# Kernel tuning notes

Hardware: AMD Instinct MI355X
Metric: run time of the kernel (lower is better)

The kernel has to match this reference:

```python
import jax, jax.numpy as jnp
import numpy as np


def setup_inputs() -> dict:
    key = jax.random.key(0)
    n_class, n_support, n_query, feature_dim = 32, 16, 16, 1024
    n_rows = n_class * n_support + n_query * n_class  # 1024
    data = jax.random.normal(key, (n_rows, feature_dim), dtype=jnp.float32)
    return {"data": data, "n_class": n_class, "n_support": n_support, "n_query": n_query}


def reference(data, n_class, n_support, n_query):
    D = data.shape[-1]
    # support: [n_class, n_support, D]; query: [n_query*n_class, D]
    support = data[: n_class * n_support].reshape(n_class, n_support, D)
    query = data[n_class * n_support :]
    # attention score: tanh(elementwise product) summed over feature dim
    # scores: [Q, n_class, n_support]  (Q = n_query*n_class)
    scores = jnp.tanh(support[None, :, :, :] * query[:, None, None, :]).sum(-1)
    att = jax.nn.softmax(scores, axis=-1)  # softmax over n_support
    # weighted instance pooling -> prototypes per (query, class): [Q, n_class, D]
    proto = jnp.einsum("qcs,csd->qcd", att, support)
    return proto
```

## Files before the change

### kernel.cpp

```cpp
#include <hip/hip_runtime.h>

constexpr int NC = 32, NS = 16, NQ = 512, D = 1024;
constexpr int QPB = 8;

__global__ __launch_bounds__(256, 2)
void proto_attn_kernel(const float* __restrict__ data, float* __restrict__ out) {
    const int c    = blockIdx.x;
    const int qt   = blockIdx.y;
    const int tid  = threadIdx.x;
    const int wave = tid >> 6;
    const int lane = tid & 63;

    __shared__ float4 sup4[NS * (D / 4)];

    const float4* sg = reinterpret_cast<const float4*>(data + (size_t)c * NS * D);
    #pragma unroll
    for (int i = 0; i < 16; ++i)
        sup4[tid + 256 * i] = sg[tid + 256 * i];
    __syncthreads();

    const float K = 2.88539008177792681472f;
    const int q0 = qt * QPB + wave * 2;
    float4 qa[4], qb[4];
    const float4* qg0 = reinterpret_cast<const float4*>(data + (size_t)(NC * NS + q0) * D);
    const float4* qg1 = reinterpret_cast<const float4*>(data + (size_t)(NC * NS + q0 + 1) * D);
    #pragma unroll
    for (int j = 0; j < 4; ++j) {
        float4 t0 = qg0[lane + 64 * j];
        float4 t1 = qg1[lane + 64 * j];
        qa[j] = make_float4(t0.x * K, t0.y * K, t0.z * K, t0.w * K);
        qb[j] = make_float4(t1.x * K, t1.y * K, t1.z * K, t1.w * K);
    }

    float sc0[NS], sc1[NS];
    #pragma unroll
    for (int s = 0; s < NS; ++s) {
        float r0 = 0.f, r1 = 0.f;
        #pragma unroll
        for (int j = 0; j < 4; ++j) {
            float4 sv = sup4[s * (D / 4) + lane + 64 * j];
            r0 += __builtin_amdgcn_rcpf(__builtin_amdgcn_exp2f(sv.x * qa[j].x) + 1.f);
            r0 += __builtin_amdgcn_rcpf(__builtin_amdgcn_exp2f(sv.y * qa[j].y) + 1.f);
            r0 += __builtin_amdgcn_rcpf(__builtin_amdgcn_exp2f(sv.z * qa[j].z) + 1.f);
            r0 += __builtin_amdgcn_rcpf(__builtin_amdgcn_exp2f(sv.w * qa[j].w) + 1.f);
            r1 += __builtin_amdgcn_rcpf(__builtin_amdgcn_exp2f(sv.x * qb[j].x) + 1.f);
            r1 += __builtin_amdgcn_rcpf(__builtin_amdgcn_exp2f(sv.y * qb[j].y) + 1.f);
            r1 += __builtin_amdgcn_rcpf(__builtin_amdgcn_exp2f(sv.z * qb[j].z) + 1.f);
            r1 += __builtin_amdgcn_rcpf(__builtin_amdgcn_exp2f(sv.w * qb[j].w) + 1.f);
        }
        #pragma unroll
        for (int m = 32; m >= 1; m >>= 1) {
            r0 += __shfl_xor(r0, m, 64);
            r1 += __shfl_xor(r1, m, 64);
        }
        sc0[s] = (float)D - 2.f * r0;
        sc1[s] = (float)D - 2.f * r1;
    }

    const float L2E = 1.44269504088896340736f;
    float m0 = sc0[0], m1 = sc1[0];
    #pragma unroll
    for (int s = 1; s < NS; ++s) { m0 = fmaxf(m0, sc0[s]); m1 = fmaxf(m1, sc1[s]); }
    float sum0 = 0.f, sum1 = 0.f;
    #pragma unroll
    for (int s = 0; s < NS; ++s) {
        sc0[s] = __builtin_amdgcn_exp2f((sc0[s] - m0) * L2E);
        sc1[s] = __builtin_amdgcn_exp2f((sc1[s] - m1) * L2E);
        sum0 += sc0[s];
        sum1 += sc1[s];
    }
    const float inv0 = __builtin_amdgcn_rcpf(sum0);
    const float inv1 = __builtin_amdgcn_rcpf(sum1);

    float4 o0[4], o1[4];
    #pragma unroll
    for (int j = 0; j < 4; ++j) {
        o0[j] = make_float4(0.f, 0.f, 0.f, 0.f);
        o1[j] = make_float4(0.f, 0.f, 0.f, 0.f);
    }
    #pragma unroll
    for (int s = 0; s < NS; ++s) {
        const float a0 = sc0[s] * inv0;
        const float a1 = sc1[s] * inv1;
        #pragma unroll
        for (int j = 0; j < 4; ++j) {
            float4 sv = sup4[s * (D / 4) + lane + 64 * j];
            o0[j].x += a0 * sv.x; o0[j].y += a0 * sv.y;
            o0[j].z += a0 * sv.z; o0[j].w += a0 * sv.w;
            o1[j].x += a1 * sv.x; o1[j].y += a1 * sv.y;
            o1[j].z += a1 * sv.z; o1[j].w += a1 * sv.w;
        }
    }
    float4* og0 = reinterpret_cast<float4*>(out + ((size_t)q0 * NC + c) * D);
    float4* og1 = reinterpret_cast<float4*>(out + ((size_t)(q0 + 1) * NC + c) * D);
    #pragma unroll
    for (int j = 0; j < 4; ++j) {
        og0[lane + 64 * j] = o0[j];
        og1[lane + 64 * j] = o1[j];
    }
}

extern "C" void kernel_launch(void* const* d_in, const int* in_sizes, int n_in,
                              void* d_out, int out_size, void* d_ws, size_t ws_size,
                              hipStream_t stream) {
    (void)in_sizes; (void)n_in; (void)out_size; (void)d_ws; (void)ws_size;
    const float* data = (const float*)d_in[0];
    float* out = (float*)d_out;
    dim3 grid(NC, NQ / QPB);
    proto_attn_kernel<<<grid, dim3(256), 0, stream>>>(data, out);
}
```

Before: 153.5 us.

## Stage support features in two halves to halve LDS and raise occupancy

Shared memory drops from 64KB to 32KB by loading the support set in two feature halves. The score pass and the pooling pass each walk both halves, so the second half is reused at the end of scoring and the first half is reloaded from global for pooling. Launch bounds rise from 2 to 4 blocks per CU to take advantage of the smaller LDS footprint. The cost is an extra global reload of half the support, plus two more block barriers. Per-lane partial sums now go into float4 accumulators before the cross-lane reduction.

```diff
diff --git a/kernel.cpp b/kernel.cpp
--- a/kernel.cpp
+++ b/kernel.cpp
@@ -2,8 +2,13 @@
 
 constexpr int NC = 32, NS = 16, NQ = 512, D = 1024;
 constexpr int QPB = 8;
+constexpr int F4H = 128;
 
-__global__ __launch_bounds__(256, 2)
+__device__ __forceinline__ float rcp1p(float t) {
+    return __builtin_amdgcn_rcpf(__builtin_amdgcn_exp2f(t) + 1.f);
+}
+
+__global__ __launch_bounds__(256, 4)
 void proto_attn_kernel(const float* __restrict__ data, float* __restrict__ out) {
     const int c    = blockIdx.x;
     const int qt   = blockIdx.y;
@@ -11,19 +16,15 @@
     const int wave = tid >> 6;
     const int lane = tid & 63;
 
-    __shared__ float4 sup4[NS * (D / 4)];
+    __shared__ float4 sup4[NS * F4H];
 
     const float4* sg = reinterpret_cast<const float4*>(data + (size_t)c * NS * D);
-    #pragma unroll
-    for (int i = 0; i < 16; ++i)
-        sup4[tid + 256 * i] = sg[tid + 256 * i];
-    __syncthreads();
 
     const float K = 2.88539008177792681472f;
     const int q0 = qt * QPB + wave * 2;
+    const float4* qg0 = reinterpret_cast<const float4*>(data + (size_t)(NC * NS + q0) * D);
+    const float4* qg1 = qg0 + 256;
     float4 qa[4], qb[4];
-    const float4* qg0 = reinterpret_cast<const float4*>(data + (size_t)(NC * NS + q0) * D);
-    const float4* qg1 = reinterpret_cast<const float4*>(data + (size_t)(NC * NS + q0 + 1) * D);
     #pragma unroll
     for (int j = 0; j < 4; ++j) {
         float4 t0 = qg0[lane + 64 * j];
@@ -32,22 +33,59 @@
         qb[j] = make_float4(t1.x * K, t1.y * K, t1.z * K, t1.w * K);
     }
 
+    #pragma unroll
+    for (int i = 0; i < 8; ++i) {
+        int idx = tid + 256 * i;
+        sup4[idx] = sg[((idx >> 7) << 8) + (idx & 127)];
+    }
+    __syncthreads();
+
     float sc0[NS], sc1[NS];
     #pragma unroll
     for (int s = 0; s < NS; ++s) {
-        float r0 = 0.f, r1 = 0.f;
+        float4 t0 = make_float4(0.f, 0.f, 0.f, 0.f);
+        float4 t1 = make_float4(0.f, 0.f, 0.f, 0.f);
         #pragma unroll
-        for (int j = 0; j < 4; ++j) {
-            float4 sv = sup4[s * (D / 4) + lane + 64 * j];
-            r0 += __builtin_amdgcn_rcpf(__builtin_amdgcn_exp2f(sv.x * qa[j].x) + 1.f);
-            r0 += __builtin_amdgcn_rcpf(__builtin_amdgcn_exp2f(sv.y * qa[j].y) + 1.f);
-            r0 += __builtin_amdgcn_rcpf(__builtin_amdgcn_exp2f(sv.z * qa[j].z) + 1.f);
-            r0 += __builtin_amdgcn_rcpf(__builtin_amdgcn_exp2f(sv.w * qa[j].w) + 1.f);
-            r1 += __builtin_amdgcn_rcpf(__builtin_amdgcn_exp2f(sv.x * qb[j].x) + 1.f);
-            r1 += __builtin_amdgcn_rcpf(__builtin_amdgcn_exp2f(sv.y * qb[j].y) + 1.f);
-            r1 += __builtin_amdgcn_rcpf(__builtin_amdgcn_exp2f(sv.z * qb[j].z) + 1.f);
-            r1 += __builtin_amdgcn_rcpf(__builtin_amdgcn_exp2f(sv.w * qb[j].w) + 1.f);
+        for (int jj = 0; jj < 2; ++jj) {
+            float4 sv = sup4[s * F4H + lane + 64 * jj];
+            float4 qA = qa[jj], qB = qb[jj];
+            t0.x += rcp1p(sv.x * qA.x); t0.y += rcp1p(sv.y * qA.y);
+            t0.z += rcp1p(sv.z * qA.z); t0.w += rcp1p(sv.w * qA.w);
+            t1.x += rcp1p(sv.x * qB.x); t1.y += rcp1p(sv.y * qB.y);
+            t1.z += rcp1p(sv.z * qB.z); t1.w += rcp1p(sv.w * qB.w);
         }
+        sc0[s] = (t0.x + t0.y) + (t0.z + t0.w);
+        sc1[s] = (t1.x + t1.y) + (t1.z + t1.w);
+    }
+    __syncthreads();
+
+    #pragma unroll
+    for (int i = 0; i < 8; ++i) {
+        int idx = tid + 256 * i;
+        sup4[idx] = sg[((idx >> 7) << 8) + 128 + (idx & 127)];
+    }
+    __syncthreads();
+
+    #pragma unroll
+    for (int s = 0; s < NS; ++s) {
+        float4 t0 = make_float4(0.f, 0.f, 0.f, 0.f);
+        float4 t1 = make_float4(0.f, 0.f, 0.f, 0.f);
+        #pragma unroll
+        for (int jj = 0; jj < 2; ++jj) {
+            float4 sv = sup4[s * F4H + lane + 64 * jj];
+            float4 qA = qa[2 + jj], qB = qb[2 + jj];
+            t0.x += rcp1p(sv.x * qA.x); t0.y += rcp1p(sv.y * qA.y);
+            t0.z += rcp1p(sv.z * qA.z); t0.w += rcp1p(sv.w * qA.w);
+            t1.x += rcp1p(sv.x * qB.x); t1.y += rcp1p(sv.y * qB.y);
+            t1.z += rcp1p(sv.z * qB.z); t1.w += rcp1p(sv.w * qB.w);
+        }
+        sc0[s] += (t0.x + t0.y) + (t0.z + t0.w);
+        sc1[s] += (t1.x + t1.y) + (t1.z + t1.w);
+    }
+
+    #pragma unroll
+    for (int s = 0; s < NS; ++s) {
+        float r0 = sc0[s], r1 = sc1[s];
         #pragma unroll
         for (int m = 32; m >= 1; m >>= 1) {
             r0 += __shfl_xor(r0, m, 64);
@@ -71,32 +109,65 @@
     }
     const float inv0 = __builtin_amdgcn_rcpf(sum0);
     const float inv1 = __builtin_amdgcn_rcpf(sum1);
+    #pragma unroll
+    for (int s = 0; s < NS; ++s) { sc0[s] *= inv0; sc1[s] *= inv1; }
 
-    float4 o0[4], o1[4];
-    #pragma unroll
-    for (int j = 0; j < 4; ++j) {
-        o0[j] = make_float4(0.f, 0.f, 0.f, 0.f);
-        o1[j] = make_float4(0.f, 0.f, 0.f, 0.f);
-    }
-    #pragma unroll
-    for (int s = 0; s < NS; ++s) {
-        const float a0 = sc0[s] * inv0;
-        const float a1 = sc1[s] * inv1;
+    float* orow0 = out + ((size_t)q0 * NC + c) * D;
+    float* orow1 = orow0 + (size_t)NC * D;
+
+    {
+        float4 o0[2], o1[2];
+        o0[0] = o0[1] = o1[0] = o1[1] = make_float4(0.f, 0.f, 0.f, 0.f);
         #pragma unroll
-        for (int j = 0; j < 4; ++j) {
-            float4 sv = sup4[s * (D / 4) + lane + 64 * j];
-            o0[j].x += a0 * sv.x; o0[j].y += a0 * sv.y;
-            o0[j].z += a0 * sv.z; o0[j].w += a0 * sv.w;
-            o1[j].x += a1 * sv.x; o1[j].y += a1 * sv.y;
-            o1[j].z += a1 * sv.z; o1[j].w += a1 * sv.w;
+        for (int s = 0; s < NS; ++s) {
+            const float a0 = sc0[s], a1 = sc1[s];
+            #pragma unroll
+            for (int jj = 0; jj < 2; ++jj) {
+                float4 sv = sup4[s * F4H + lane + 64 * jj];
+                o0[jj].x += a0 * sv.x; o0[jj].y += a0 * sv.y;
+                o0[jj].z += a0 * sv.z; o0[jj].w += a0 * sv.w;
+                o1[jj].x += a1 * sv.x; o1[jj].y += a1 * sv.y;
+                o1[jj].z += a1 * sv.z; o1[jj].w += a1 * sv.w;
+            }
+        }
+        float4* og0 = reinterpret_cast<float4*>(orow0) + 128;
+        float4* og1 = reinterpret_cast<float4*>(orow1) + 128;
+        #pragma unroll
+        for (int jj = 0; jj < 2; ++jj) {
+            og0[lane + 64 * jj] = o0[jj];
+            og1[lane + 64 * jj] = o1[jj];
         }
     }
-    float4* og0 = reinterpret_cast<float4*>(out + ((size_t)q0 * NC + c) * D);
-    float4* og1 = reinterpret_cast<float4*>(out + ((size_t)(q0 + 1) * NC + c) * D);
+    __syncthreads();
+
     #pragma unroll
-    for (int j = 0; j < 4; ++j) {
-        og0[lane + 64 * j] = o0[j];
-        og1[lane + 64 * j] = o1[j];
+    for (int i = 0; i < 8; ++i) {
+        int idx = tid + 256 * i;
+        sup4[idx] = sg[((idx >> 7) << 8) + (idx & 127)];
+    }
+    __syncthreads();
+    {
+        float4 o0[2], o1[2];
+        o0[0] = o0[1] = o1[0] = o1[1] = make_float4(0.f, 0.f, 0.f, 0.f);
+        #pragma unroll
+        for (int s = 0; s < NS; ++s) {
+            const float a0 = sc0[s], a1 = sc1[s];
+            #pragma unroll
+            for (int jj = 0; jj < 2; ++jj) {
+                float4 sv = sup4[s * F4H + lane + 64 * jj];
+                o0[jj].x += a0 * sv.x; o0[jj].y += a0 * sv.y;
+                o0[jj].z += a0 * sv.z; o0[jj].w += a0 * sv.w;
+                o1[jj].x += a1 * sv.x; o1[jj].y += a1 * sv.y;
+                o1[jj].z += a1 * sv.z; o1[jj].w += a1 * sv.w;
+            }
+        }
+        float4* og0 = reinterpret_cast<float4*>(orow0);
+        float4* og1 = reinterpret_cast<float4*>(orow1);
+        #pragma unroll
+        for (int jj = 0; jj < 2; ++jj) {
+            og0[lane + 64 * jj] = o0[jj];
+            og1[lane + 64 * jj] = o1[jj];
+        }
     }
 }
 
```

Measured after the change: 149.7 us. -2.4%, faster.

## Pair sigmoid reciprocals, read support from global, batch wave reductions

Applied to the files above, without the earlier changes.

Replaces two reciprocals per element pair with one by computing 1/x+1/y as (x+y)/(xy), cutting transcendental-unit work in the tanh-sum loop. It also drops the 64KB shared-memory staging of the support set and its barrier, reading support rows straight from global/L2. Cross-lane shuffle reductions are moved into a separate loop after all partial sums are computed. Costs include more global load traffic per wave, since the support set is now read by every wave in both passes, and a possible overflow risk in x*y for large exponents.

```diff
diff --git a/kernel.cpp b/kernel.cpp
--- a/kernel.cpp
+++ b/kernel.cpp
@@ -2,6 +2,12 @@
 
 constexpr int NC = 32, NS = 16, NQ = 512, D = 1024;
 constexpr int QPB = 8;
+
+__device__ __forceinline__ float pair_term(float t0, float t1) {
+    float x = __builtin_amdgcn_exp2f(t0) + 1.f;
+    float y = __builtin_amdgcn_exp2f(t1) + 1.f;
+    return (x + y) * __builtin_amdgcn_rcpf(x * y);
+}
 
 __global__ __launch_bounds__(256, 2)
 void proto_attn_kernel(const float* __restrict__ data, float* __restrict__ out) {
@@ -11,19 +17,13 @@
     const int wave = tid >> 6;
     const int lane = tid & 63;
 
-    __shared__ float4 sup4[NS * (D / 4)];
-
     const float4* sg = reinterpret_cast<const float4*>(data + (size_t)c * NS * D);
-    #pragma unroll
-    for (int i = 0; i < 16; ++i)
-        sup4[tid + 256 * i] = sg[tid + 256 * i];
-    __syncthreads();
 
     const float K = 2.88539008177792681472f;
     const int q0 = qt * QPB + wave * 2;
+    const float4* qg0 = reinterpret_cast<const float4*>(data + (size_t)(NC * NS + q0) * D);
+    const float4* qg1 = qg0 + 256;
     float4 qa[4], qb[4];
-    const float4* qg0 = reinterpret_cast<const float4*>(data + (size_t)(NC * NS + q0) * D);
-    const float4* qg1 = reinterpret_cast<const float4*>(data + (size_t)(NC * NS + q0 + 1) * D);
     #pragma unroll
     for (int j = 0; j < 4; ++j) {
         float4 t0 = qg0[lane + 64 * j];
@@ -35,19 +35,23 @@
     float sc0[NS], sc1[NS];
     #pragma unroll
     for (int s = 0; s < NS; ++s) {
-        float r0 = 0.f, r1 = 0.f;
+        float u0 = 0.f, v0 = 0.f, u1 = 0.f, v1 = 0.f;
         #pragma unroll
         for (int j = 0; j < 4; ++j) {
-            float4 sv = sup4[s * (D / 4) + lane + 64 * j];
-            r0 += __builtin_amdgcn_rcpf(__builtin_amdgcn_exp2f(sv.x * qa[j].x) + 1.f);
-            r0 += __builtin_amdgcn_rcpf(__builtin_amdgcn_exp2f(sv.y * qa[j].y) + 1.f);
-            r0 += __builtin_amdgcn_rcpf(__builtin_amdgcn_exp2f(sv.z * qa[j].z) + 1.f);
-            r0 += __builtin_amdgcn_rcpf(__builtin_amdgcn_exp2f(sv.w * qa[j].w) + 1.f);
-            r1 += __builtin_amdgcn_rcpf(__builtin_amdgcn_exp2f(sv.x * qb[j].x) + 1.f);
-            r1 += __builtin_amdgcn_rcpf(__builtin_amdgcn_exp2f(sv.y * qb[j].y) + 1.f);
-            r1 += __builtin_amdgcn_rcpf(__builtin_amdgcn_exp2f(sv.z * qb[j].z) + 1.f);
-            r1 += __builtin_amdgcn_rcpf(__builtin_amdgcn_exp2f(sv.w * qb[j].w) + 1.f);
+            float4 sv = sg[s * 256 + lane + 64 * j];
+            float4 qA = qa[j], qB = qb[j];
+            u0 += pair_term(sv.x * qA.x, sv.y * qA.y);
+            v0 += pair_term(sv.z * qA.z, sv.w * qA.w);
+            u1 += pair_term(sv.x * qB.x, sv.y * qB.y);
+            v1 += pair_term(sv.z * qB.z, sv.w * qB.w);
         }
+        sc0[s] = u0 + v0;
+        sc1[s] = u1 + v1;
+    }
+
+    #pragma unroll
+    for (int s = 0; s < NS; ++s) {
+        float r0 = sc0[s], r1 = sc1[s];
         #pragma unroll
         for (int m = 32; m >= 1; m >>= 1) {
             r0 += __shfl_xor(r0, m, 64);
@@ -71,6 +75,8 @@
     }
     const float inv0 = __builtin_amdgcn_rcpf(sum0);
     const float inv1 = __builtin_amdgcn_rcpf(sum1);
+    #pragma unroll
+    for (int s = 0; s < NS; ++s) { sc0[s] *= inv0; sc1[s] *= inv1; }
 
     float4 o0[4], o1[4];
     #pragma unroll
@@ -80,11 +86,10 @@
     }
     #pragma unroll
     for (int s = 0; s < NS; ++s) {
-        const float a0 = sc0[s] * inv0;
-        const float a1 = sc1[s] * inv1;
+        const float a0 = sc0[s], a1 = sc1[s];
         #pragma unroll
         for (int j = 0; j < 4; ++j) {
-            float4 sv = sup4[s * (D / 4) + lane + 64 * j];
+            float4 sv = sg[s * 256 + lane + 64 * j];
             o0[j].x += a0 * sv.x; o0[j].y += a0 * sv.y;
             o0[j].z += a0 * sv.z; o0[j].w += a0 * sv.w;
             o1[j].x += a1 * sv.x; o1[j].y += a1 * sv.y;
```

Measured after the change: 180.0 us. 17.3% more time.
